# Kernel optimization log

Hardware: AMD Instinct MI355X
Metric: run time of the kernel (lower is better)

Reference implementation:

```python
import jax, jax.numpy as jnp
import numpy as np

N_NODES = 50000
N_EDGES = 800000
C = 64
N_STEPS = 4
N_MIX = 14  # sum_{i=0..3} (i+2)
NEG_SLOPE = 0.2  # PyG GATConv default negative_slope


def setup_inputs() -> dict:
    key = jax.random.key(0)
    ks = jax.random.split(key, 9)
    g = lambda k, shp: jax.random.normal(k, shp, jnp.float32) * (1.0 / np.sqrt(C))
    return {
        "x": jax.random.normal(ks[0], (N_NODES, C), jnp.float32),
        "edge_index": jax.random.randint(ks[1], (2, N_EDGES), 0, N_NODES, dtype=jnp.int64),
        "alphas": jax.random.normal(ks[2], (N_MIX, 5), jnp.float32),
        "gcn_W": g(ks[3], (N_MIX, C, C)),
        "gcn_b": jnp.zeros((N_MIX, C), jnp.float32),
        "sage_Wl": g(ks[4], (N_MIX, C, C)),
        "sage_Wr": g(ks[5], (N_MIX, C, C)),
        "sage_b": jnp.zeros((N_MIX, C), jnp.float32),
        "gat_W": g(ks[6], (N_MIX, C, C)),
        "gat_a_src": g(ks[7], (N_MIX, C)),
        "gat_a_dst": g(ks[8], (N_MIX, C)),
        "gat_b": jnp.zeros((N_MIX, C), jnp.float32),
    }


def _cell(x, edge_index, alphas, gcn_W, gcn_b, sage_Wl, sage_Wr, sage_b,
          gat_W, gat_a_src, gat_a_dst, gat_b):
    n = x.shape[0]
    src, dst = edge_index[0], edge_index[1]
    loop = jnp.arange(n)
    # edges with self-loops (used by GCN and GAT, per PyG defaults)
    src_sl = jnp.concatenate([src, loop])
    dst_sl = jnp.concatenate([dst, loop])

    # GCN symmetric normalization: deg over self-looped targets, norm per edge.
    deg = jax.ops.segment_sum(jnp.ones(src_sl.shape, jnp.float32), dst_sl, num_segments=n)
    dinv = jnp.where(deg > 0, jax.lax.rsqrt(deg), 0.0)
    gcn_norm = dinv[src_sl] * dinv[dst_sl]  # [E+N]

    # SAGE mean-aggregation denominator (no self loops; empty -> clamp to 1, sum is 0 anyway)
    cnt = jnp.maximum(
        jax.ops.segment_sum(jnp.ones(dst.shape, jnp.float32), dst, num_segments=n), 1.0)

    def gcn(h, k):
        hw = h @ gcn_W[k]  # [n, C]
        return jax.ops.segment_sum(gcn_norm[:, None] * hw[src_sl], dst_sl,
                                   num_segments=n) + gcn_b[k]

    def sage(h, k):
        agg = jax.ops.segment_sum(h[src], dst, num_segments=n) / cnt[:, None]
        return agg @ sage_Wl[k] + h @ sage_Wr[k] + sage_b[k]

    def gat(h, k):
        hw = h @ gat_W[k]  # shared lin for src/dst (same node set)
        e = (hw @ gat_a_src[k])[src_sl] + (hw @ gat_a_dst[k])[dst_sl]
        e = jnp.where(e > 0, e, NEG_SLOPE * e)  # LeakyReLU
        # segment softmax over incoming edges per target (self-loops make all segments non-empty)
        emax = jax.ops.segment_max(e, dst_sl, num_segments=n)
        ee = jnp.exp(e - emax[dst_sl])
        denom = jax.ops.segment_sum(ee, dst_sl, num_segments=n)
        a = ee / denom[dst_sl]
        return jax.ops.segment_sum(a[:, None] * hw[src_sl], dst_sl,
                                   num_segments=n) + gat_b[k]

    def mixed(h, k):
        w = jax.nn.softmax(alphas[k])  # [5]: gcn, sage, gat, identity, zero
        return w[0] * gcn(h, k) + w[1] * sage(h, k) + w[2] * gat(h, k) + w[3] * h

    states = [x, x]
    offset = 0
    for i in range(N_STEPS):
        s = 0.0
        for j in range(i + 2):
            s = s + mixed(states[j], offset + j)
        offset += i + 2
        states.append(s)
    return jnp.mean(jnp.stack(states[-N_STEPS:], axis=0), axis=0)


def reference(x, edge_index, alphas, gcn_W, gcn_b, sage_Wl, sage_Wr, sage_b,
              gat_W, gat_a_src, gat_a_dst, gat_b):
    return _cell(x, edge_index, alphas, gcn_W, gcn_b, sage_Wl, sage_Wr, sage_b,
                 gat_W, gat_a_src, gat_a_dst, gat_b)
```

## Files before the change

### kernel.cpp

```cpp
#include <hip/hip_runtime.h>

#define N_NODES 50000
#define N_EDGES 800000
#define CCH 64
#define N_MIX 14
#define NBUCK 196
#define BCAP 6144
#define ECHUNK 3125
#define DBINS 64

typedef __bf16 bf16x8 __attribute__((ext_vector_type(8)));
typedef float floatx4 __attribute__((ext_vector_type(4)));

__device__ __forceinline__ float leaky(float x) {
    return fmaxf(x, 0.2f * x);
}

__global__ void prep_weights(const float* __restrict__ alphas,
                             const float* __restrict__ gcn_W, const float* __restrict__ gcn_b,
                             const float* __restrict__ sage_Wl, const float* __restrict__ sage_Wr,
                             const float* __restrict__ sage_b, const float* __restrict__ gat_Wp,
                             const float* __restrict__ a_src, const float* __restrict__ a_dst,
                             const float* __restrict__ gat_b,
                             __bf16* __restrict__ Wt, float* __restrict__ bc,
                             float* __restrict__ vs, float* __restrict__ vd) {
    int k = blockIdx.x;
    __shared__ float w[5];
    if (threadIdx.x == 0) {
        float a[5], m = -1e30f, s = 0.f;
        for (int i = 0; i < 5; ++i) { a[i] = alphas[k * 5 + i]; m = fmaxf(m, a[i]); }
        for (int i = 0; i < 5; ++i) { a[i] = __expf(a[i] - m); s += a[i]; }
        for (int i = 0; i < 5; ++i) w[i] = a[i] / s;
    }
    __syncthreads();
    float gamma = (k >= 9) ? 0.25f : 1.0f;
    float w0 = gamma * w[0], w1 = gamma * w[1], w2 = gamma * w[2], w3 = gamma * w[3];
    float idext = (k >= 11) ? 0.25f : 0.f;
    for (int idx = threadIdx.x; idx < 64 * 256; idx += blockDim.x) {
        int c = idx >> 8, j = idx & 255;
        float v;
        if (j < 64)       v = w0 * gcn_W[k * 4096 + j * 64 + c];
        else if (j < 128) v = w1 * sage_Wl[k * 4096 + (j - 64) * 64 + c];
        else if (j < 192) {
            int jj = j - 128;
            v = w1 * sage_Wr[k * 4096 + jj * 64 + c];
            if (jj == c) v += w3 + idext;
        } else {
            v = w2 * gat_Wp[k * 4096 + (j - 192) * 64 + c];
        }
        Wt[(size_t)k * 16384 + idx] = (__bf16)v;
    }
    if (threadIdx.x < 64) {
        int r = threadIdx.x;
        bc[k * 64 + r] = gamma * (w[0] * gcn_b[k * 64 + r] + w[1] * sage_b[k * 64 + r] +
                                  w[2] * gat_b[k * 64 + r]);
        float s1 = 0.f, s2 = 0.f;
        for (int j = 0; j < 64; ++j) {
            float wv_ = gat_Wp[k * 4096 + r * 64 + j];
            s1 += wv_ * a_src[k * 64 + j];
            s2 += wv_ * a_dst[k * 64 + j];
        }
        vs[k * 64 + r] = s1;
        vd[k * 64 + r] = s2;
    }
}

__global__ void prep_scoreV(const float* __restrict__ vs, const float* __restrict__ vd,
                            __bf16* __restrict__ Vph,
                            unsigned km0, unsigned km1, unsigned km2, unsigned km3,
                            unsigned nks) {
    int p = blockIdx.x;
    unsigned km = (p == 0) ? km0 : (p == 1) ? km1 : (p == 2) ? km2 : km3;
    int nk = (nks >> (p * 4)) & 15;
    for (int idx = threadIdx.x; idx < 1024; idx += blockDim.x) {
        int n = idx >> 6, kk = idx & 63;
        int t = n & 7;
        float v = 0.f;
        if (t < nk) {
            int k = (km >> (4 * t)) & 15;
            v = (n < 8) ? vs[k * 64 + kk] : vd[k * 64 + kk];
        }
        Vph[p * 1024 + n * 64 + kk] = (__bf16)v;
    }
}

__global__ void convert_bf16(const float4* __restrict__ src, __bf16* __restrict__ dst, int n4) {
    int i = blockIdx.x * blockDim.x + threadIdx.x;
    if (i < n4) {
        float4 v = src[i];
        dst[i * 4 + 0] = (__bf16)v.x;
        dst[i * 4 + 1] = (__bf16)v.y;
        dst[i * 4 + 2] = (__bf16)v.z;
        dst[i * 4 + 3] = (__bf16)v.w;
    }
}

__global__ __launch_bounds__(256) void bucket_count(const int* __restrict__ ei,
                                                    int* __restrict__ bcount) {
    __shared__ int h[NBUCK];
    for (int i = threadIdx.x; i < NBUCK; i += 256) h[i] = 0;
    __syncthreads();
    int e0 = blockIdx.x * ECHUNK;
    for (int i = threadIdx.x; i < ECHUNK; i += 256)
        atomicAdd(&h[ei[N_EDGES + e0 + i] >> 8], 1);
    __syncthreads();
    for (int i = threadIdx.x; i < NBUCK; i += 256)
        if (h[i]) atomicAdd(&bcount[i], h[i]);
}

__global__ __launch_bounds__(256) void bucket_scan(const int* __restrict__ bcount,
                                                   int* __restrict__ bbase,
                                                   int* __restrict__ row_ptr) {
    __shared__ int s[256];
    int t = threadIdx.x;
    int v = (t < NBUCK) ? bcount[t] : 0;
    s[t] = v;
    __syncthreads();
    for (int o = 1; o < 256; o <<= 1) {
        int t2 = (t >= o) ? s[t - o] : 0;
        __syncthreads();
        s[t] += t2;
        __syncthreads();
    }
    if (t < NBUCK) bbase[t + 1] = s[t];
    if (t == 0) { bbase[0] = 0; row_ptr[N_NODES] = N_EDGES; }
}

__global__ __launch_bounds__(256) void bucket_scatter(const int* __restrict__ ei,
                                                      const int* __restrict__ bbase,
                                                      int* __restrict__ bfill,
                                                      unsigned* __restrict__ pairs) {
    __shared__ int lh[NBUCK], lbase[NBUCK], lcur[NBUCK];
    int tid = threadIdx.x;
    int e0 = blockIdx.x * ECHUNK;
    for (int i = tid; i < NBUCK; i += 256) { lh[i] = 0; lcur[i] = 0; }
    __syncthreads();
    for (int i = tid; i < ECHUNK; i += 256)
        atomicAdd(&lh[ei[N_EDGES + e0 + i] >> 8], 1);
    __syncthreads();
    for (int i = tid; i < NBUCK; i += 256)
        lbase[i] = bbase[i] + ((lh[i] > 0) ? atomicAdd(&bfill[i], lh[i]) : 0);
    __syncthreads();
    for (int i = tid; i < ECHUNK; i += 256) {
        int s = ei[e0 + i];
        int d = ei[N_EDGES + e0 + i];
        int b = d >> 8;
        int pos = atomicAdd(&lcur[b], 1);
        pairs[lbase[b] + pos] = (unsigned)s | ((unsigned)(d & 255) << 16);
    }
}

__global__ __launch_bounds__(256) void bucket_sort(const unsigned* __restrict__ pairs,
                                                   const int* __restrict__ bbase,
                                                   int* __restrict__ row_ptr,
                                                   int* __restrict__ col_idx,
                                                   float* __restrict__ dinv,
                                                   float* __restrict__ cntf) {
    int b = blockIdx.x;
    __shared__ unsigned buf[BCAP];
    __shared__ int hist[256], off[256], cur[256];
    int tid = threadIdx.x;
    hist[tid] = 0;
    __syncthreads();
    int base = bbase[b], cnt = bbase[b + 1] - base;
    if (cnt > BCAP) cnt = BCAP;
    for (int i = tid; i < cnt; i += 256) {
        unsigned pr = pairs[(size_t)base + i];
        buf[i] = pr;
        atomicAdd(&hist[(pr >> 16) & 255], 1);
    }
    __syncthreads();
    int v = hist[tid];
    off[tid] = v;
    __syncthreads();
    for (int o = 1; o < 256; o <<= 1) {
        int t2 = (tid >= o) ? off[tid - o] : 0;
        __syncthreads();
        off[tid] += t2;
        __syncthreads();
    }
    int excl = off[tid] - v;
    int node = b * 256 + tid;
    if (node < N_NODES) {
        row_ptr[node] = base + excl;
        dinv[node] = rsqrtf((float)(v + 1));
        cntf[node] = (float)(v > 0 ? v : 1);
    }
    cur[tid] = excl;
    __syncthreads();
    for (int i = tid; i < cnt; i += 256) {
        unsigned pr = buf[i];
        int ln = (pr >> 16) & 255;
        int pos = atomicAdd(&cur[ln], 1);
        col_idx[base + pos] = (int)(pr & 0xffffu);
    }
}

__global__ __launch_bounds__(256) void deg_hist(const int* __restrict__ row_ptr,
                                                int* __restrict__ dh) {
    __shared__ int h[DBINS];
    if (threadIdx.x < DBINS) h[threadIdx.x] = 0;
    __syncthreads();
    int i = blockIdx.x * 256 + threadIdx.x;
    if (i < N_NODES) {
        int d = row_ptr[i + 1] - row_ptr[i];
        atomicAdd(&h[min(d, DBINS - 1)], 1);
    }
    __syncthreads();
    if (threadIdx.x < DBINS && h[threadIdx.x]) atomicAdd(&dh[threadIdx.x], h[threadIdx.x]);
}

__global__ __launch_bounds__(64) void deg_scan(const int* __restrict__ dh,
                                               int* __restrict__ dbase) {
    int t = threadIdx.x;
    int v = dh[t];
    int inc = v;
#pragma unroll
    for (int o = 1; o < 64; o <<= 1) {
        int t2 = __shfl_up(inc, o, 64);
        if (t >= o) inc += t2;
    }
    dbase[t] = inc - v;
}

__global__ __launch_bounds__(256) void deg_scatter(const int* __restrict__ row_ptr,
                                                   const int* __restrict__ dbase,
                                                   int* __restrict__ dfill,
                                                   int* __restrict__ perm) {
    __shared__ int lh[DBINS], lbase[DBINS], lcur[DBINS];
    int tid = threadIdx.x;
    if (tid < DBINS) { lh[tid] = 0; lcur[tid] = 0; }
    __syncthreads();
    int i = blockIdx.x * 256 + tid;
    int d = -1;
    if (i < N_NODES) {
        d = min(row_ptr[i + 1] - row_ptr[i], DBINS - 1);
        atomicAdd(&lh[d], 1);
    }
    __syncthreads();
    if (tid < DBINS) lbase[tid] = dbase[tid] + ((lh[tid] > 0) ? atomicAdd(&dfill[tid], lh[tid]) : 0);
    __syncthreads();
    if (i < N_NODES) {
        int pos = lbase[d] + atomicAdd(&lcur[d], 1);
        perm[pos] = i;
    }
}

__global__ __launch_bounds__(256) void score_mfma(const __bf16* __restrict__ hb,
                                                  const __bf16* __restrict__ V,
                                                  float* __restrict__ ssrcS,
                                                  float* __restrict__ sdstS) {
    int tid = threadIdx.x;
    int wave = tid >> 6, lane = tid & 63;
    int quad = lane >> 4, mr = lane & 15;
    int r0 = blockIdx.x * 128 + wave * 32;
    bf16x8 b0 = *(const bf16x8*)(V + mr * 64 + (quad << 3));
    bf16x8 b1 = *(const bf16x8*)(V + mr * 64 + 32 + (quad << 3));
#pragma unroll
    for (int rt = 0; rt < 2; ++rt) {
        int r = r0 + rt * 16 + mr;
        if (r > N_NODES - 1) r = N_NODES - 1;
        bf16x8 a0 = *(const bf16x8*)(hb + (size_t)r * 64 + (quad << 3));
        bf16x8 a1 = *(const bf16x8*)(hb + (size_t)r * 64 + 32 + (quad << 3));
        floatx4 acc = (floatx4){0.f, 0.f, 0.f, 0.f};
        acc = __builtin_amdgcn_mfma_f32_16x16x32_bf16(a0, b0, acc, 0, 0, 0);
        acc = __builtin_amdgcn_mfma_f32_16x16x32_bf16(a1, b1, acc, 0, 0, 0);
#pragma unroll
        for (int reg = 0; reg < 4; ++reg) {
            int row = r0 + rt * 16 + quad * 4 + reg;
            if (row < N_NODES) {
                if (mr < 8) ssrcS[(size_t)row * 8 + mr] = acc[reg];
                else        sdstS[(size_t)row * 8 + (mr - 8)] = acc[reg];
            }
        }
    }
}

template <int NK>
__global__ __launch_bounds__(128, 4) void fused_gather(
    const __bf16* __restrict__ hb, const int* __restrict__ row_ptr,
    const int* __restrict__ col_idx, const float* __restrict__ dinv,
    const float* __restrict__ cntf, const float* __restrict__ ssrcS,
    const float* __restrict__ sdstS, const int* __restrict__ perm,
    int soff, int doGS,
    __bf16* __restrict__ aggG, __bf16* __restrict__ aggS, __bf16* __restrict__ A) {
    int wid = blockIdx.x * 2 + (threadIdx.x >> 6);
    int lane = threadIdx.x & 63;
    int sub = lane >> 3, ln = lane & 7;
    int node = perm[wid * 8 + sub];
    int beg = row_ptr[node], end = row_ptr[node + 1];

    float sd[NK], selfraw[NK];
    {
        float svv[8], dvl[8];
        float4 a0 = *(const float4*)(ssrcS + (size_t)node * 8 + soff);
        float4 b0 = *(const float4*)(sdstS + (size_t)node * 8 + soff);
        svv[0] = a0.x; svv[1] = a0.y; svv[2] = a0.z; svv[3] = a0.w;
        dvl[0] = b0.x; dvl[1] = b0.y; dvl[2] = b0.z; dvl[3] = b0.w;
        if (NK > 4) {
            float4 a1 = *(const float4*)(ssrcS + (size_t)node * 8 + soff + 4);
            float4 b1 = *(const float4*)(sdstS + (size_t)node * 8 + soff + 4);
            svv[4] = a1.x; svv[5] = a1.y; svv[6] = a1.z; svv[7] = a1.w;
            dvl[4] = b1.x; dvl[5] = b1.y; dvl[6] = b1.z; dvl[7] = b1.w;
        }
#pragma unroll
        for (int t = 0; t < NK; ++t) {
            sd[t] = dvl[t];
            selfraw[t] = leaky(svv[t] + sd[t]);
        }
    }
    bf16x8 hsb = *(const bf16x8*)(hb + (size_t)node * 64 + ln * 8);
    float hs[8];
#pragma unroll
    for (int c = 0; c < 8; ++c) hs[c] = (float)hsb[c];

    float denoml[NK], acc[NK][8], accG[8], accS[8];
#pragma unroll
    for (int c = 0; c < 8; ++c) { accG[c] = 0.f; accS[c] = 0.f; }
#pragma unroll
    for (int t = 0; t < NK; ++t) {
        denoml[t] = 0.f;
#pragma unroll
        for (int c = 0; c < 8; ++c) acc[t][c] = hs[c];
    }
    for (int base = beg; base < end; base += 8) {
        int e = base + ln;
        int col = 0;
        float dv = 0.f, wv[NK];
#pragma unroll
        for (int t = 0; t < NK; ++t) wv[t] = 0.f;
        if (e < end) {
            col = col_idx[e];
            dv = dinv[col];
            float svv[8];
            float4 a0 = *(const float4*)(ssrcS + (size_t)col * 8 + soff);
            svv[0] = a0.x; svv[1] = a0.y; svv[2] = a0.z; svv[3] = a0.w;
            if (NK > 4) {
                float4 a1 = *(const float4*)(ssrcS + (size_t)col * 8 + soff + 4);
                svv[4] = a1.x; svv[5] = a1.y; svv[6] = a1.z; svv[7] = a1.w;
            }
#pragma unroll
            for (int t = 0; t < NK; ++t) {
                wv[t] = __expf(leaky(svv[t] + sd[t]) - selfraw[t]);
                denoml[t] += wv[t];
            }
        }
        int jcnt = end - base;
        if (jcnt > 8) jcnt = 8;
        int cs0 = __shfl(col, (sub << 3), 64);
        bf16x8 hx = *(const bf16x8*)(hb + (size_t)cs0 * 64 + ln * 8);
        for (int j = 0; j < jcnt; ++j) {
            bf16x8 hxn;
            if (j + 1 < jcnt) {
                int csn = __shfl(col, (sub << 3) | (j + 1), 64);
                hxn = *(const bf16x8*)(hb + (size_t)csn * 64 + ln * 8);
            }
            int srcl = (sub << 3) | j;
            float dvj = __shfl(dv, srcl, 64);
            float wj[NK];
#pragma unroll
            for (int t = 0; t < NK; ++t) wj[t] = __shfl(wv[t], srcl, 64);
#pragma unroll
            for (int c = 0; c < 8; ++c) {
                float f = (float)hx[c];
                accS[c] += f;
                accG[c] += dvj * f;
#pragma unroll
                for (int t = 0; t < NK; ++t) acc[t][c] += wj[t] * f;
            }
            hx = hxn;
        }
    }
    float denom[NK];
#pragma unroll
    for (int t = 0; t < NK; ++t) {
        float w = denoml[t];
#pragma unroll
        for (int off = 1; off < 8; off <<= 1) w += __shfl_xor(w, off, 64);
        denom[t] = w + 1.0f;
    }

    if (doGS) {
        float dvn = dinv[node];
        float cin = 1.0f / cntf[node];
        bf16x8 og, os;
#pragma unroll
        for (int c = 0; c < 8; ++c) {
            os[c] = (__bf16)(accS[c] * cin);
            og[c] = (__bf16)(dvn * accG[c] + dvn * dvn * hs[c]);
        }
        *(bf16x8*)(aggS + (size_t)node * 64 + ln * 8) = os;
        *(bf16x8*)(aggG + (size_t)node * 64 + ln * 8) = og;
    }
#pragma unroll
    for (int t = 0; t < NK; ++t) {
        bf16x8 oa;
        float inv = 1.0f / denom[t];
#pragma unroll
        for (int c = 0; c < 8; ++c) oa[c] = (__bf16)(acc[t][c] * inv);
        *(bf16x8*)(A + (size_t)t * N_NODES * 64 + (size_t)node * 64 + ln * 8) = oa;
    }
}

struct GArgs {
    const __bf16* G;
    const __bf16* S;
    const __bf16* Hb;
    const __bf16* A0;
    const __bf16* Wt;
    const float* bc;
    __bf16* tgb[3];
    float* tgf;
    long long slot;
    int nk;
    int initmask;
    int kidx[8];
    int tsel[8];
};

__global__ __launch_bounds__(256) void gemm_group(GArgs a) {
    __shared__ __bf16 Wl[64 * 264];
    int tid = threadIdx.x;
    int wave = tid >> 6, lane = tid & 63;
    int quad = lane >> 4, mr = lane & 15;
    int r0 = blockIdx.x * 128 + wave * 32;
    bf16x8 gf[2][2], sf[2][2], hf[2][2];
#pragma unroll
    for (int rt = 0; rt < 2; ++rt) {
        int r = r0 + rt * 16 + mr;
        if (r > N_NODES - 1) r = N_NODES - 1;
#pragma unroll
        for (int hh = 0; hh < 2; ++hh) {
            int colj = hh * 32 + (quad << 3);
            gf[rt][hh] = *(const bf16x8*)(a.G + (size_t)r * 64 + colj);
            sf[rt][hh] = *(const bf16x8*)(a.S + (size_t)r * 64 + colj);
            hf[rt][hh] = *(const bf16x8*)(a.Hb + (size_t)r * 64 + colj);
        }
    }
    floatx4 acc[2][4];
    float bsum[4];
#pragma unroll
    for (int rt = 0; rt < 2; ++rt)
#pragma unroll
        for (int ct = 0; ct < 4; ++ct) acc[rt][ct] = (floatx4){0.f, 0.f, 0.f, 0.f};
#pragma unroll
    for (int ct = 0; ct < 4; ++ct) bsum[ct] = 0.f;
    int runstart = 0;
    for (int t = 0; t < a.nk; ++t) {
        int k = a.kidx[t];
        __syncthreads();
        {
            const uint4* src = (const uint4*)(a.Wt + (size_t)k * 16384);
            for (int i = tid; i < 2048; i += 256) {
                int row = i >> 5, colj = (i & 31) << 3;
                *(uint4*)&Wl[row * 264 + colj] = src[i];
            }
        }
        __syncthreads();
        const __bf16* Ap = a.A0 + (size_t)t * a.slot;
        bf16x8 af[2][2];
#pragma unroll
        for (int rt = 0; rt < 2; ++rt) {
            int r = r0 + rt * 16 + mr;
            if (r > N_NODES - 1) r = N_NODES - 1;
#pragma unroll
            for (int hh = 0; hh < 2; ++hh)
                af[rt][hh] = *(const bf16x8*)(Ap + (size_t)r * 64 + hh * 32 + (quad << 3));
        }
        const float* bp = a.bc + k * 64;
#pragma unroll
        for (int ct = 0; ct < 4; ++ct) bsum[ct] += bp[ct * 16 + mr];
#pragma unroll
        for (int seg = 0; seg < 4; ++seg) {
#pragma unroll
            for (int hh = 0; hh < 2; ++hh) {
                int kt = seg * 2 + hh;
                bf16x8 a0 = (seg == 0) ? gf[0][hh] : (seg == 1) ? sf[0][hh]
                            : (seg == 2) ? hf[0][hh] : af[0][hh];
                bf16x8 a1 = (seg == 0) ? gf[1][hh] : (seg == 1) ? sf[1][hh]
                            : (seg == 2) ? hf[1][hh] : af[1][hh];
#pragma unroll
                for (int ct = 0; ct < 4; ++ct) {
                    bf16x8 bfr = *(const bf16x8*)&Wl[(ct * 16 + mr) * 264 + (kt << 5) + (quad << 3)];
                    acc[0][ct] = __builtin_amdgcn_mfma_f32_16x16x32_bf16(a0, bfr, acc[0][ct], 0, 0, 0);
                    acc[1][ct] = __builtin_amdgcn_mfma_f32_16x16x32_bf16(a1, bfr, acc[1][ct], 0, 0, 0);
                }
            }
        }
        bool flush = (t == a.nk - 1) || (a.tsel[t + 1] != a.tsel[t]);
        if (flush) {
            int ts = a.tsel[t];
            int init = (a.initmask >> runstart) & 1;
            if (ts < 3) {
                __bf16* tgt = a.tgb[ts];
#pragma unroll
                for (int rt = 0; rt < 2; ++rt) {
#pragma unroll
                    for (int reg = 0; reg < 4; ++reg) {
                        int r = r0 + rt * 16 + quad * 4 + reg;
                        if (r < N_NODES) {
#pragma unroll
                            for (int ct = 0; ct < 4; ++ct) {
                                int c = ct * 16 + mr;
                                float v = acc[rt][ct][reg] + bsum[ct];
                                size_t idx = (size_t)r * 64 + c;
                                if (!init) v += (float)tgt[idx];
                                tgt[idx] = (__bf16)v;
                            }
                        }
                    }
                }
            } else {
                float* tgt = a.tgf;
#pragma unroll
                for (int rt = 0; rt < 2; ++rt) {
#pragma unroll
                    for (int reg = 0; reg < 4; ++reg) {
                        int r = r0 + rt * 16 + quad * 4 + reg;
                        if (r < N_NODES) {
#pragma unroll
                            for (int ct = 0; ct < 4; ++ct) {
                                int c = ct * 16 + mr;
                                float v = acc[rt][ct][reg] + bsum[ct];
                                size_t idx = (size_t)r * 64 + c;
                                if (!init) v += tgt[idx];
                                tgt[idx] = v;
                            }
                        }
                    }
                }
            }
#pragma unroll
            for (int rt = 0; rt < 2; ++rt)
#pragma unroll
                for (int ct = 0; ct < 4; ++ct) acc[rt][ct] = (floatx4){0.f, 0.f, 0.f, 0.f};
#pragma unroll
            for (int ct = 0; ct < 4; ++ct) bsum[ct] = 0.f;
            runstart = t + 1;
        }
    }
}

extern "C" void kernel_launch(void* const* d_in, const int* in_sizes, int n_in,
                              void* d_out, int out_size, void* d_ws, size_t ws_size,
                              hipStream_t stream) {
    const float* x       = (const float*)d_in[0];
    const int*   ei      = (const int*)d_in[1];
    const float* alphas  = (const float*)d_in[2];
    const float* gcn_W   = (const float*)d_in[3];
    const float* gcn_b   = (const float*)d_in[4];
    const float* sage_Wl = (const float*)d_in[5];
    const float* sage_Wr = (const float*)d_in[6];
    const float* sage_b  = (const float*)d_in[7];
    const float* gat_W   = (const float*)d_in[8];
    const float* a_src   = (const float*)d_in[9];
    const float* a_dst   = (const float*)d_in[10];
    const float* gat_b   = (const float*)d_in[11];
    float* out = (float*)d_out;

    char* p = (char*)d_ws;
    auto alloc = [&](size_t bytes) -> char* {
        char* r = p;
        p += (bytes + 255) & ~(size_t)255;
        return r;
    };
    const size_t NCf = (size_t)N_NODES * CCH;
    const size_t NC16 = NCf * 2;
    __bf16* hbuf[4];
    for (int i = 0; i < 4; ++i) hbuf[i] = (__bf16*)alloc(NC16);
    __bf16* aggG = (__bf16*)alloc(NC16);
    __bf16* aggS = (__bf16*)alloc(NC16);
    float* ssrcS = (float*)alloc((size_t)N_NODES * 8 * 4);
    float* sdstS = (float*)alloc((size_t)N_NODES * 8 * 4);
    float* dinv  = (float*)alloc(N_NODES * 4);
    float* cntf  = (float*)alloc(N_NODES * 4);
    int* row_ptr = (int*)alloc((N_NODES + 1) * 4);
    int* col_idx = (int*)alloc((size_t)N_EDGES * 4);
    unsigned* pairs = (unsigned*)alloc((size_t)N_EDGES * 4);
    int* bcount  = (int*)alloc(NBUCK * 4);
    int* bfill   = (int*)alloc(NBUCK * 4);
    int* bbase   = (int*)alloc((NBUCK + 1) * 4);
    int* dh      = (int*)alloc(DBINS * 4);
    int* dbase   = (int*)alloc(DBINS * 4);
    int* dfill   = (int*)alloc(DBINS * 4);
    int* perm    = (int*)alloc(N_NODES * 4);
    __bf16* Wt   = (__bf16*)alloc((size_t)N_MIX * 16384 * 2);
    float* bcv   = (float*)alloc(N_MIX * 64 * 4);
    float* vs    = (float*)alloc(N_MIX * 64 * 4);
    float* vd    = (float*)alloc(N_MIX * 64 * 4);
    __bf16* Vph  = (__bf16*)alloc(4 * 1024 * 2);

    size_t used = (size_t)(p - (char*)d_ws);
    int navail = (int)((ws_size > used) ? ((ws_size - used) / NC16) : 0);
    if (navail < 1) navail = 1;
    if (navail > 8) navail = 8;
    __bf16* Abuf = (__bf16*)alloc((size_t)navail * NC16);

    hipMemsetAsync(bcount, 0, NBUCK * 4, stream);
    hipMemsetAsync(bfill, 0, NBUCK * 4, stream);
    hipMemsetAsync(dh, 0, DBINS * 4, stream);
    hipMemsetAsync(dfill, 0, DBINS * 4, stream);

    prep_weights<<<N_MIX, 256, 0, stream>>>(alphas, gcn_W, gcn_b, sage_Wl, sage_Wr, sage_b,
                                            gat_W, a_src, a_dst, gat_b, Wt, bcv, vs, vd);
    prep_scoreV<<<4, 256, 0, stream>>>(vs, vd, Vph, 0xA9653210u, 0xB74u, 0xC8u, 0xDu, 0x1238u);
    convert_bf16<<<(int)((NCf / 4 + 255) / 256), 256, 0, stream>>>((const float4*)x, hbuf[0],
                                                                   (int)(NCf / 4));
    bucket_count<<<256, 256, 0, stream>>>(ei, bcount);
    bucket_scan<<<1, 256, 0, stream>>>(bcount, bbase, row_ptr);
    bucket_scatter<<<256, 256, 0, stream>>>(ei, bbase, bfill, pairs);
    bucket_sort<<<NBUCK, 256, 0, stream>>>(pairs, bbase, row_ptr, col_idx, dinv, cntf);
    deg_hist<<<NBUCK, 256, 0, stream>>>(row_ptr, dh);
    deg_scan<<<1, 64, 0, stream>>>(dh, dbase);
    deg_scatter<<<NBUCK, 256, 0, stream>>>(row_ptr, dbase, dfill, perm);

    const int AGG_GRID = N_NODES / 16;
    const int GEMM_GRID = (N_NODES + 127) / 128;

    struct Phase { int nk; int ks[8]; int tg[8]; };
    const Phase ph[4] = {
        {8, {0, 1, 2, 3, 5, 6, 9, 10}, {0, 0, 1, 1, 2, 2, 3, 3}},
        {3, {4, 7, 11, 0, 0, 0, 0, 0}, {1, 2, 3, 0, 0, 0, 0, 0}},
        {2, {8, 12, 0, 0, 0, 0, 0, 0}, {2, 3, 0, 0, 0, 0, 0, 0}},
        {1, {13, 0, 0, 0, 0, 0, 0, 0}, {3, 0, 0, 0, 0, 0, 0, 0}},
    };

    auto launch_gather = [&](int nkk, const __bf16* hb, int soff, int doGS, __bf16* Aslot) {
        switch (nkk) {
            case 8: fused_gather<8><<<AGG_GRID, 128, 0, stream>>>(hb, row_ptr, col_idx, dinv, cntf, ssrcS, sdstS, perm, soff, doGS, aggG, aggS, Aslot); break;
            case 4: fused_gather<4><<<AGG_GRID, 128, 0, stream>>>(hb, row_ptr, col_idx, dinv, cntf, ssrcS, sdstS, perm, soff, doGS, aggG, aggS, Aslot); break;
            case 3: fused_gather<3><<<AGG_GRID, 128, 0, stream>>>(hb, row_ptr, col_idx, dinv, cntf, ssrcS, sdstS, perm, soff, doGS, aggG, aggS, Aslot); break;
            case 2: fused_gather<2><<<AGG_GRID, 128, 0, stream>>>(hb, row_ptr, col_idx, dinv, cntf, ssrcS, sdstS, perm, soff, doGS, aggG, aggS, Aslot); break;
            default: fused_gather<1><<<AGG_GRID, 128, 0, stream>>>(hb, row_ptr, col_idx, dinv, cntf, ssrcS, sdstS, perm, soff, doGS, aggG, aggS, Aslot); break;
        }
    };
    auto make_gemm = [&](const Phase& P, const __bf16* hb, int kstart, int g) {
        GArgs ga;
        ga.G = aggG; ga.S = aggS; ga.Hb = hb; ga.A0 = Abuf;
        ga.Wt = Wt; ga.bc = bcv;
        ga.tgb[0] = hbuf[1]; ga.tgb[1] = hbuf[2]; ga.tgb[2] = hbuf[3];
        ga.tgf = out;
        ga.slot = (long long)NCf;
        ga.nk = g;
        ga.initmask = 0;
        for (int j = 0; j < g; ++j) {
            int k = P.ks[kstart + j];
            ga.kidx[j] = k;
            ga.tsel[j] = P.tg[kstart + j];
            if (k == 0 || k == 2 || k == 5 || k == 9) ga.initmask |= (1 << j);
        }
        for (int j = g; j < 8; ++j) { ga.kidx[j] = 0; ga.tsel[j] = (j > 0) ? ga.tsel[j - 1] : 0; }
        gemm_group<<<GEMM_GRID, 256, 0, stream>>>(ga);
    };

    for (int st = 0; st < 4; ++st) {
        const Phase& P = ph[st];
        const __bf16* hb = hbuf[st];
        score_mfma<<<GEMM_GRID, 256, 0, stream>>>(hb, Vph + st * 1024, ssrcS, sdstS);
        if (navail >= P.nk) {
            launch_gather(P.nk, hb, 0, 1, Abuf);
            make_gemm(P, hb, 0, P.nk);
        } else {
            int gs = (navail < 4) ? navail : 4;
            for (int done = 0; done < P.nk;) {
                int g = gs;
                if (g > P.nk - done) g = P.nk - done;
                launch_gather(g, hb, done, (done == 0) ? 1 : 0, Abuf);
                make_gemm(P, hb, done, g);
                done += g;
            }
        }
    }
}
```

Measured before the change: 466.2 us.

## Fuse degree sort into bucket_sort, halve GEMM row tile, relax gather launch bounds

The global degree-histogram, scan and scatter kernels are folded into bucket_sort, which now builds a degree-sorted perm locally within each 256-node bucket, removing three launches and two memsets. The gemm_group kernel now handles 16 rows per wave instead of 32, doubling its grid to raise occupancy and cut register use, at the cost of reloading the shared weights more often. fused_gather with more than four kernels gets a lower minimum-blocks hint so it has more registers. The per-bucket sort changes load balance compared with a global degree sort.

```diff
diff --git a/kernel.cpp b/kernel.cpp
--- a/kernel.cpp
+++ b/kernel.cpp
@@ -7,7 +7,6 @@
 #define NBUCK 196
 #define BCAP 6144
 #define ECHUNK 3125
-#define DBINS 64
 
 typedef __bf16 bf16x8 __attribute__((ext_vector_type(8)));
 typedef float floatx4 __attribute__((ext_vector_type(4)));
@@ -155,12 +154,15 @@
                                                    int* __restrict__ row_ptr,
                                                    int* __restrict__ col_idx,
                                                    float* __restrict__ dinv,
-                                                   float* __restrict__ cntf) {
+                                                   float* __restrict__ cntf,
+                                                   int* __restrict__ perm) {
     int b = blockIdx.x;
     __shared__ unsigned buf[BCAP];
     __shared__ int hist[256], off[256], cur[256];
+    __shared__ int dh2[64], dbase2[64], dcur2[64];
     int tid = threadIdx.x;
     hist[tid] = 0;
+    if (tid < 64) { dh2[tid] = 0; dcur2[tid] = 0; }
     __syncthreads();
     int base = bbase[b], cnt = bbase[b + 1] - base;
     if (cnt > BCAP) cnt = BCAP;
@@ -181,68 +183,36 @@
     }
     int excl = off[tid] - v;
     int node = b * 256 + tid;
+    int dbin = -1;
     if (node < N_NODES) {
         row_ptr[node] = base + excl;
         dinv[node] = rsqrtf((float)(v + 1));
         cntf[node] = (float)(v > 0 ? v : 1);
+        dbin = min(v, 63);
+        atomicAdd(&dh2[dbin], 1);
     }
     cur[tid] = excl;
     __syncthreads();
+    if (tid < 64) {
+        int val = dh2[tid];
+        int inc = val;
+#pragma unroll
+        for (int o = 1; o < 64; o <<= 1) {
+            int t2 = __shfl_up(inc, o, 64);
+            if (tid >= o) inc += t2;
+        }
+        dbase2[tid] = inc - val;
+    }
+    __syncthreads();
+    if (node < N_NODES) {
+        int pos = dbase2[dbin] + atomicAdd(&dcur2[dbin], 1);
+        perm[b * 256 + pos] = node;
+    }
     for (int i = tid; i < cnt; i += 256) {
         unsigned pr = buf[i];
         int ln = (pr >> 16) & 255;
         int pos = atomicAdd(&cur[ln], 1);
         col_idx[base + pos] = (int)(pr & 0xffffu);
-    }
-}
-
-__global__ __launch_bounds__(256) void deg_hist(const int* __restrict__ row_ptr,
-                                                int* __restrict__ dh) {
-    __shared__ int h[DBINS];
-    if (threadIdx.x < DBINS) h[threadIdx.x] = 0;
-    __syncthreads();
-    int i = blockIdx.x * 256 + threadIdx.x;
-    if (i < N_NODES) {
-        int d = row_ptr[i + 1] - row_ptr[i];
-        atomicAdd(&h[min(d, DBINS - 1)], 1);
-    }
-    __syncthreads();
-    if (threadIdx.x < DBINS && h[threadIdx.x]) atomicAdd(&dh[threadIdx.x], h[threadIdx.x]);
-}
-
-__global__ __launch_bounds__(64) void deg_scan(const int* __restrict__ dh,
-                                               int* __restrict__ dbase) {
-    int t = threadIdx.x;
-    int v = dh[t];
-    int inc = v;
-#pragma unroll
-    for (int o = 1; o < 64; o <<= 1) {
-        int t2 = __shfl_up(inc, o, 64);
-        if (t >= o) inc += t2;
-    }
-    dbase[t] = inc - v;
-}
-
-__global__ __launch_bounds__(256) void deg_scatter(const int* __restrict__ row_ptr,
-                                                   const int* __restrict__ dbase,
-                                                   int* __restrict__ dfill,
-                                                   int* __restrict__ perm) {
-    __shared__ int lh[DBINS], lbase[DBINS], lcur[DBINS];
-    int tid = threadIdx.x;
-    if (tid < DBINS) { lh[tid] = 0; lcur[tid] = 0; }
-    __syncthreads();
-    int i = blockIdx.x * 256 + tid;
-    int d = -1;
-    if (i < N_NODES) {
-        d = min(row_ptr[i + 1] - row_ptr[i], DBINS - 1);
-        atomicAdd(&lh[d], 1);
-    }
-    __syncthreads();
-    if (tid < DBINS) lbase[tid] = dbase[tid] + ((lh[tid] > 0) ? atomicAdd(&dfill[tid], lh[tid]) : 0);
-    __syncthreads();
-    if (i < N_NODES) {
-        int pos = lbase[d] + atomicAdd(&lcur[d], 1);
-        perm[pos] = i;
     }
 }
 
@@ -277,7 +247,7 @@
 }
 
 template <int NK>
-__global__ __launch_bounds__(128, 4) void fused_gather(
+__global__ __launch_bounds__(128, (NK > 4 ? 2 : 4)) void fused_gather(
     const __bf16* __restrict__ hb, const int* __restrict__ row_ptr,
     const int* __restrict__ col_idx, const float* __restrict__ dinv,
     const float* __restrict__ cntf, const float* __restrict__ ssrcS,
@@ -423,28 +393,21 @@
     int tid = threadIdx.x;
     int wave = tid >> 6, lane = tid & 63;
     int quad = lane >> 4, mr = lane & 15;
-    int r0 = blockIdx.x * 128 + wave * 32;
-    bf16x8 gf[2][2], sf[2][2], hf[2][2];
-#pragma unroll
-    for (int rt = 0; rt < 2; ++rt) {
-        int r = r0 + rt * 16 + mr;
-        if (r > N_NODES - 1) r = N_NODES - 1;
-#pragma unroll
-        for (int hh = 0; hh < 2; ++hh) {
-            int colj = hh * 32 + (quad << 3);
-            gf[rt][hh] = *(const bf16x8*)(a.G + (size_t)r * 64 + colj);
-            sf[rt][hh] = *(const bf16x8*)(a.S + (size_t)r * 64 + colj);
-            hf[rt][hh] = *(const bf16x8*)(a.Hb + (size_t)r * 64 + colj);
-        }
-    }
-    floatx4 acc[2][4];
+    int r0 = blockIdx.x * 64 + wave * 16;
+    int r = r0 + mr;
+    if (r > N_NODES - 1) r = N_NODES - 1;
+    bf16x8 gf[2], sf[2], hf[2];
+#pragma unroll
+    for (int hh = 0; hh < 2; ++hh) {
+        int colj = hh * 32 + (quad << 3);
+        gf[hh] = *(const bf16x8*)(a.G + (size_t)r * 64 + colj);
+        sf[hh] = *(const bf16x8*)(a.S + (size_t)r * 64 + colj);
+        hf[hh] = *(const bf16x8*)(a.Hb + (size_t)r * 64 + colj);
+    }
+    floatx4 acc[4];
     float bsum[4];
 #pragma unroll
-    for (int rt = 0; rt < 2; ++rt)
-#pragma unroll
-        for (int ct = 0; ct < 4; ++ct) acc[rt][ct] = (floatx4){0.f, 0.f, 0.f, 0.f};
-#pragma unroll
-    for (int ct = 0; ct < 4; ++ct) bsum[ct] = 0.f;
+    for (int ct = 0; ct < 4; ++ct) { acc[ct] = (floatx4){0.f, 0.f, 0.f, 0.f}; bsum[ct] = 0.f; }
     int runstart = 0;
     for (int t = 0; t < a.nk; ++t) {
         int k = a.kidx[t];
@@ -458,15 +421,10 @@
         }
         __syncthreads();
         const __bf16* Ap = a.A0 + (size_t)t * a.slot;
-        bf16x8 af[2][2];
-#pragma unroll
-        for (int rt = 0; rt < 2; ++rt) {
-            int r = r0 + rt * 16 + mr;
-            if (r > N_NODES - 1) r = N_NODES - 1;
-#pragma unroll
-            for (int hh = 0; hh < 2; ++hh)
-                af[rt][hh] = *(const bf16x8*)(Ap + (size_t)r * 64 + hh * 32 + (quad << 3));
-        }
+        bf16x8 af[2];
+#pragma unroll
+        for (int hh = 0; hh < 2; ++hh)
+            af[hh] = *(const bf16x8*)(Ap + (size_t)r * 64 + hh * 32 + (quad << 3));
         const float* bp = a.bc + k * 64;
 #pragma unroll
         for (int ct = 0; ct < 4; ++ct) bsum[ct] += bp[ct * 16 + mr];
@@ -475,15 +433,12 @@
 #pragma unroll
             for (int hh = 0; hh < 2; ++hh) {
                 int kt = seg * 2 + hh;
-                bf16x8 a0 = (seg == 0) ? gf[0][hh] : (seg == 1) ? sf[0][hh]
-                            : (seg == 2) ? hf[0][hh] : af[0][hh];
-                bf16x8 a1 = (seg == 0) ? gf[1][hh] : (seg == 1) ? sf[1][hh]
-                            : (seg == 2) ? hf[1][hh] : af[1][hh];
+                bf16x8 a0 = (seg == 0) ? gf[hh] : (seg == 1) ? sf[hh]
+                            : (seg == 2) ? hf[hh] : af[hh];
 #pragma unroll
                 for (int ct = 0; ct < 4; ++ct) {
                     bf16x8 bfr = *(const bf16x8*)&Wl[(ct * 16 + mr) * 264 + (kt << 5) + (quad << 3)];
-                    acc[0][ct] = __builtin_amdgcn_mfma_f32_16x16x32_bf16(a0, bfr, acc[0][ct], 0, 0, 0);
-                    acc[1][ct] = __builtin_amdgcn_mfma_f32_16x16x32_bf16(a1, bfr, acc[1][ct], 0, 0, 0);
+                    acc[ct] = __builtin_amdgcn_mfma_f32_16x16x32_bf16(a0, bfr, acc[ct], 0, 0, 0);
                 }
             }
         }
@@ -494,48 +449,38 @@
             if (ts < 3) {
                 __bf16* tgt = a.tgb[ts];
 #pragma unroll
-                for (int rt = 0; rt < 2; ++rt) {
-#pragma unroll
-                    for (int reg = 0; reg < 4; ++reg) {
-                        int r = r0 + rt * 16 + quad * 4 + reg;
-                        if (r < N_NODES) {
-#pragma unroll
-                            for (int ct = 0; ct < 4; ++ct) {
-                                int c = ct * 16 + mr;
-                                float v = acc[rt][ct][reg] + bsum[ct];
-                                size_t idx = (size_t)r * 64 + c;
-                                if (!init) v += (float)tgt[idx];
-                                tgt[idx] = (__bf16)v;
-                            }
+                for (int reg = 0; reg < 4; ++reg) {
+                    int row = r0 + quad * 4 + reg;
+                    if (row < N_NODES) {
+#pragma unroll
+                        for (int ct = 0; ct < 4; ++ct) {
+                            int c = ct * 16 + mr;
+                            float v = acc[ct][reg] + bsum[ct];
+                            size_t idx = (size_t)row * 64 + c;
+                            if (!init) v += (float)tgt[idx];
+                            tgt[idx] = (__bf16)v;
                         }
                     }
                 }
             } else {
                 float* tgt = a.tgf;
 #pragma unroll
-                for (int rt = 0; rt < 2; ++rt) {
-#pragma unroll
-                    for (int reg = 0; reg < 4; ++reg) {
-                        int r = r0 + rt * 16 + quad * 4 + reg;
-                        if (r < N_NODES) {
-#pragma unroll
-                            for (int ct = 0; ct < 4; ++ct) {
-                                int c = ct * 16 + mr;
-                                float v = acc[rt][ct][reg] + bsum[ct];
-                                size_t idx = (size_t)r * 64 + c;
-                                if (!init) v += tgt[idx];
-                                tgt[idx] = v;
-                            }
+                for (int reg = 0; reg < 4; ++reg) {
+                    int row = r0 + quad * 4 + reg;
+                    if (row < N_NODES) {
+#pragma unroll
+                        for (int ct = 0; ct < 4; ++ct) {
+                            int c = ct * 16 + mr;
+                            float v = acc[ct][reg] + bsum[ct];
+                            size_t idx = (size_t)row * 64 + c;
+                            if (!init) v += tgt[idx];
+                            tgt[idx] = v;
                         }
                     }
                 }
             }
 #pragma unroll
-            for (int rt = 0; rt < 2; ++rt)
-#pragma unroll
-                for (int ct = 0; ct < 4; ++ct) acc[rt][ct] = (floatx4){0.f, 0.f, 0.f, 0.f};
-#pragma unroll
-            for (int ct = 0; ct < 4; ++ct) bsum[ct] = 0.f;
+            for (int ct = 0; ct < 4; ++ct) { acc[ct] = (floatx4){0.f, 0.f, 0.f, 0.f}; bsum[ct] = 0.f; }
             runstart = t + 1;
         }
     }
@@ -580,9 +525,6 @@
     int* bcount  = (int*)alloc(NBUCK * 4);
     int* bfill   = (int*)alloc(NBUCK * 4);
     int* bbase   = (int*)alloc((NBUCK + 1) * 4);
-    int* dh      = (int*)alloc(DBINS * 4);
-    int* dbase   = (int*)alloc(DBINS * 4);
-    int* dfill   = (int*)alloc(DBINS * 4);
     int* perm    = (int*)alloc(N_NODES * 4);
     __bf16* Wt   = (__bf16*)alloc((size_t)N_MIX * 16384 * 2);
     float* bcv   = (float*)alloc(N_MIX * 64 * 4);
@@ -598,8 +540,6 @@
 
     hipMemsetAsync(bcount, 0, NBUCK * 4, stream);
     hipMemsetAsync(bfill, 0, NBUCK * 4, stream);
-    hipMemsetAsync(dh, 0, DBINS * 4, stream);
-    hipMemsetAsync(dfill, 0, DBINS * 4, stream);
 
     prep_weights<<<N_MIX, 256, 0, stream>>>(alphas, gcn_W, gcn_b, sage_Wl, sage_Wr, sage_b,
                                             gat_W, a_src, a_dst, gat_b, Wt, bcv, vs, vd);
@@ -609,13 +549,11 @@
     bucket_count<<<256, 256, 0, stream>>>(ei, bcount);
     bucket_scan<<<1, 256, 0, stream>>>(bcount, bbase, row_ptr);
     bucket_scatter<<<256, 256, 0, stream>>>(ei, bbase, bfill, pairs);
-    bucket_sort<<<NBUCK, 256, 0, stream>>>(pairs, bbase, row_ptr, col_idx, dinv, cntf);
-    deg_hist<<<NBUCK, 256, 0, stream>>>(row_ptr, dh);
-    deg_scan<<<1, 64, 0, stream>>>(dh, dbase);
-    deg_scatter<<<NBUCK, 256, 0, stream>>>(row_ptr, dbase, dfill, perm);
+    bucket_sort<<<NBUCK, 256, 0, stream>>>(pairs, bbase, row_ptr, col_idx, dinv, cntf, perm);
 
     const int AGG_GRID = N_NODES / 16;
-    const int GEMM_GRID = (N_NODES + 127) / 128;
+    const int SCORE_GRID = (N_NODES + 127) / 128;
+    const int GEMM_GRID = (N_NODES + 63) / 64;
 
     struct Phase { int nk; int ks[8]; int tg[8]; };
     const Phase ph[4] = {
@@ -656,7 +594,7 @@
     for (int st = 0; st < 4; ++st) {
         const Phase& P = ph[st];
         const __bf16* hb = hbuf[st];
-        score_mfma<<<GEMM_GRID, 256, 0, stream>>>(hb, Vph + st * 1024, ssrcS, sdstS);
+        score_mfma<<<SCORE_GRID, 256, 0, stream>>>(hb, Vph + st * 1024, ssrcS, sdstS);
         if (navail >= P.nk) {
             launch_gather(P.nk, hb, 0, 1, Abuf);
             make_gemm(P, hb, 0, P.nk);
```

Result: faster. 443.6 us (-4.8%).
